# Kernel tuning notes

Hardware: AMD Instinct MI355X
Metric: run time of the kernel (lower is better)

## Reference

```python
import jax, jax.numpy as jnp
import numpy as np
from jax import lax

B, L, D_MODEL = 2, 4096, 1024
D_INNER = 2 * D_MODEL          # expand=2
D_STATE = D_INNER              # required: complex einsum contracts d_inner vs d_state
DT_RANK = 64                   # ceil(1024/16)
D_CONV = 4


def setup_inputs() -> dict:
    key = jax.random.key(0)
    ks = jax.random.split(key, 16)
    s = lambda *sh: 1.0 / np.sqrt(sh[-1])
    return {
        "hidden_states": jax.random.normal(ks[0], (B, L, D_MODEL), jnp.float32),
        "delta": jax.random.normal(ks[1], (B, L, DT_RANK), jnp.float32),
        # in_proj: Linear(d_model -> 2*d_inner), no bias
        "in_proj_w": jax.random.normal(ks[2], (2 * D_INNER, D_MODEL), jnp.float32) * s(D_MODEL),
        # depthwise causal conv1d: (out=d_inner, in/groups=1, k)
        "conv_w": jax.random.normal(ks[3], (D_INNER, 1, D_CONV), jnp.float32) * s(D_CONV),
        "conv_b": jax.random.normal(ks[4], (D_INNER,), jnp.float32) * 0.01,
        # ComplexStateSpace: only A_real affects the real output (x is real)
        "A_real": jax.random.normal(ks[5], (D_STATE, D_STATE), jnp.float32) * 0.1 / np.sqrt(D_STATE),
        # MIMO linears (torch Linear weight layout [out, in])
        "B_w": jax.random.normal(ks[6], (D_STATE, D_INNER), jnp.float32) * 0.1 * s(D_INNER),
        "C_w": jax.random.normal(ks[7], (D_INNER, D_STATE), jnp.float32) * 0.1 * s(D_STATE),
        "D_w": jax.random.normal(ks[8], (D_INNER, D_INNER), jnp.float32) * 0.1 * s(D_INNER),
        # SelectiveScan params
        "dt_proj_w": jax.random.normal(ks[9], (D_INNER, DT_RANK), jnp.float32) * 0.01,
        "dt_proj_b": jax.random.normal(ks[10], (D_INNER,), jnp.float32) * 0.01,
        "A_log": jax.random.uniform(ks[11], (D_INNER,), jnp.float32, -4.0, -1.0),
        "D_ss": jnp.ones((D_INNER,), jnp.float32),
        # out_proj: Linear(d_inner -> d_model), no bias
        "out_proj_w": jax.random.normal(ks[12], (D_MODEL, D_INNER), jnp.float32) * s(D_INNER),
    }


def reference(hidden_states, delta, in_proj_w, conv_w, conv_b, A_real,
              B_w, C_w, D_w, dt_proj_w, dt_proj_b, A_log, D_ss, out_proj_w):
    d_inner = A_log.shape[0]
    # in_proj + split
    xz = jnp.einsum('bld,ed->ble', hidden_states, in_proj_w)
    x, z = xz[..., :d_inner], xz[..., d_inner:]
    # depthwise causal conv1d (left-pad k-1 == torch pad both + truncate to L)
    xc = jnp.swapaxes(x, 1, 2)                      # [b, d, l]
    xc = lax.conv_general_dilated(xc, conv_w, window_strides=(1,),
                                  padding=[(D_CONV - 1, 0)],
                                  feature_group_count=d_inner)
    x = jnp.swapaxes(xc, 1, 2) + conv_b             # [b, l, d]
    x = jax.nn.silu(x)
    # ComplexStateSpace: real part of (x @ (A_real + iA_imag)) == x @ A_real
    x = x + jnp.einsum('bls,st->blt', x, A_real)
    # MIMO SSM: state_t = cumsum(B x)_t ; y_t = C state_t + D x_t  (vectorized)
    Bx = jnp.einsum('bld,sd->bls', x, B_w)          # [b, l, d_state]
    states = jnp.cumsum(Bx, axis=1)
    x_mimo = jnp.einsum('bls,es->ble', states, C_w) + jnp.einsum('bld,ed->ble', x, D_w)
    x = x + x_mimo
    # SelectiveScan: state = state * exp(dlt * A) + u, A = -exp(A_log)
    dlt = jax.nn.softplus(jnp.einsum('blr,dr->bld', delta, dt_proj_w) + dt_proj_b)
    decay = jnp.exp(dlt * (-jnp.exp(A_log)))        # [b, l, d], in (0, 1)

    def step(state, inp):
        dec, u = inp
        state = state * dec + u
        return state, state

    init = jnp.zeros_like(x[:, 0])
    _, scan_states = lax.scan(step, init,
                              (jnp.swapaxes(decay, 0, 1), jnp.swapaxes(x, 0, 1)))
    x = jnp.swapaxes(scan_states, 0, 1) + x * D_ss
    # gate + out projection
    out = x * jax.nn.silu(z)
    return jnp.einsum('ble,de->bld', out, out_proj_w)
```

## Files before the change

kernel.cpp:

```cpp
#include <hip/hip_runtime.h>
#include <cstdint>
#include <cstddef>


typedef unsigned short u16;
typedef __bf16 bf16x8 __attribute__((ext_vector_type(8)));
typedef float  f32x4  __attribute__((ext_vector_type(4)));

#define BDIM 256
#define M_ROWS 8192
#define LSEQ   4096
#define DI     2048
#define NCH    64
#define CLEN   64

__device__ __forceinline__ float bf2f(u16 h) {
    return __uint_as_float(((unsigned int)h) << 16);
}
__device__ __forceinline__ u16 f2bf(float f) {
    unsigned int u = __float_as_uint(f);
    u = u + 0x7fffu + ((u >> 16) & 1u);
    return (u16)(u >> 16);
}
__device__ __forceinline__ float siluf(float v) { return v / (1.0f + __expf(-v)); }

__device__ __forceinline__ void load16_to_lds(const u16* g, u16* l) {
    __builtin_amdgcn_global_load_lds((const __attribute__((address_space(1))) void*)g,
                                     (__attribute__((address_space(3))) void*)l,
                                     16, 0, 0);
}

__global__ void k_cvt_all(const float* __restrict__ hs, const float* __restrict__ inproj,
                          const float* __restrict__ Bw, const float* __restrict__ Cw,
                          const float* __restrict__ outw, const float* __restrict__ delta,
                          const float* __restrict__ dtw, const float* __restrict__ Areal,
                          const float* __restrict__ Dw, const float* __restrict__ Alog,
                          u16* __restrict__ XH, u16* __restrict__ W1, u16* __restrict__ WBb,
                          u16* __restrict__ WC, u16* __restrict__ WO, u16* __restrict__ DLT,
                          u16* __restrict__ WDT, u16* __restrict__ Pb, u16* __restrict__ Db,
                          float* __restrict__ NA) {
    long i = (long)(blockIdx.x * BDIM + threadIdx.x) * 4;
    if (i >= 32112640L) {
        long j = i - 32112640L;
        if (j < 2048) {
            float4 v = *reinterpret_cast<const float4*>(Alog + j);
            float4 o = {-__expf(v.x), -__expf(v.y), -__expf(v.z), -__expf(v.w)};
            *reinterpret_cast<float4*>(NA + j) = o;
        }
        return;
    }
    const float* src; u16* dst; long off; bool diag = false;
    if      (i <  8388608L) { src = hs;     dst = XH;  off = 0L; }
    else if (i < 12582912L) { src = inproj; dst = W1;  off = 8388608L; }
    else if (i < 16777216L) { src = Bw;     dst = WBb; off = 12582912L; }
    else if (i < 20971520L) { src = Cw;     dst = WC;  off = 16777216L; }
    else if (i < 23068672L) { src = outw;   dst = WO;  off = 20971520L; }
    else if (i < 23592960L) { src = delta;  dst = DLT; off = 23068672L; }
    else if (i < 23724032L) { src = dtw;    dst = WDT; off = 23592960L; }
    else if (i < 27918336L) { src = Areal;  dst = Pb;  off = 23724032L; diag = true; }
    else                    { src = Dw;     dst = Db;  off = 27918336L; diag = true; }
    long j = i - off;
    float4 v = *reinterpret_cast<const float4*>(src + j);
    if (diag) {
        int r = (int)(j >> 11), c = (int)(j & 2047);
        if (r >= c && r < c + 4) (&v.x)[r - c] += 1.0f;
    }
    ushort2 a = {f2bf(v.x), f2bf(v.y)};
    ushort2 b = {f2bf(v.z), f2bf(v.w)};
    *reinterpret_cast<ushort2*>(dst + j)     = a;
    *reinterpret_cast<ushort2*>(dst + j + 2) = b;
}

__device__ __forceinline__ void gemm_core(
    u16* As, u16* Bs,
    const u16* __restrict__ A1, const u16* __restrict__ W1, int K1,
    const u16* __restrict__ A2, const u16* __restrict__ W2, int K2,
    int N, float* __restrict__ outf, u16* __restrict__ outb, u16* __restrict__ outb2,
    const float* __restrict__ bias1, const float* __restrict__ bias2,
    int m0, int n0, int mode) {
    const int tid  = threadIdx.x;
    const int wave = tid >> 6;
    const int lane = tid & 63;
    const int wm = (wave >> 1) * 64;
    const int wn = (wave & 1) * 64;
    const int lr = lane & 15;
    const int lq = lane >> 4;
    const int stg_row = lane >> 3;
    const int stg_col = (((lane & 7) ^ (lane >> 3)) << 3);

    f32x4 acc[4][4] = {};

    const int nt1 = K1 >> 6;
    const int nt2 = K2 >> 6;
    const int ntot = nt1 + nt2;

    for (int kt = 0; kt < ntot; ++kt) {
        const u16* Ap; const u16* Wp; int ld, k0;
        if (kt < nt1) { Ap = A1; Wp = W1; ld = K1; k0 = kt << 6; }
        else          { Ap = A2; Wp = W2; ld = K2; k0 = (kt - nt1) << 6; }
        #pragma unroll
        for (int i = 0; i < 4; ++i) {
            int chunk = wave * 4 + i;
            int r = chunk * 8 + stg_row;
            load16_to_lds(Ap + (size_t)(m0 + r) * ld + (k0 + stg_col), As + chunk * 512);
            load16_to_lds(Wp + (size_t)(n0 + r) * ld + (k0 + stg_col), Bs + chunk * 512);
        }
        __syncthreads();
        #pragma unroll
        for (int kk = 0; kk < 64; kk += 32) {
            bf16x8 af[4], bfr[4];
            #pragma unroll
            for (int i = 0; i < 4; ++i) {
                int R = wm + i * 16 + lr;
                af[i] = *reinterpret_cast<const bf16x8*>(
                    &As[R * 64 + ((kk + lq * 8) ^ ((R & 7) << 3))]);
            }
            #pragma unroll
            for (int i = 0; i < 4; ++i) {
                int R = wn + i * 16 + lr;
                bfr[i] = *reinterpret_cast<const bf16x8*>(
                    &Bs[R * 64 + ((kk + lq * 8) ^ ((R & 7) << 3))]);
            }
            #pragma unroll
            for (int mi = 0; mi < 4; ++mi)
                #pragma unroll
                for (int ni = 0; ni < 4; ++ni)
                    acc[mi][ni] = __builtin_amdgcn_mfma_f32_16x16x32_bf16(
                        af[mi], bfr[ni], acc[mi][ni], 0, 0, 0);
        }
        __syncthreads();
    }

    if (mode == 8) {
        #pragma unroll
        for (int mi = 0; mi < 4; ++mi) {
            #pragma unroll
            for (int ni = 0; ni < 4; ++ni) {
                int row = m0 + wm + mi * 16 + lq * 4;
                int col = n0 + wn + ni * 16 + lr;
                ushort4 v;
                v.x = f2bf(acc[mi][ni][0]); v.y = f2bf(acc[mi][ni][1]);
                v.z = f2bf(acc[mi][ni][2]); v.w = f2bf(acc[mi][ni][3]);
                *reinterpret_cast<ushort4*>(outb + (size_t)col * 2048 + row) = v;
            }
        }
        return;
    }

    #pragma unroll
    for (int mi = 0; mi < 4; ++mi) {
        #pragma unroll
        for (int ni = 0; ni < 4; ++ni) {
            #pragma unroll
            for (int j = 0; j < 4; ++j) {
                int row = m0 + wm + mi * 16 + lq * 4 + j;
                int col = n0 + wn + ni * 16 + lr;
                float v = acc[mi][ni][j];
                if (mode == 6) {
                    if (col < 2048) outb [(size_t)row * 2048 + col]        = f2bf(v);
                    else            outb2[(size_t)row * 2048 + col - 2048] = f2bf(v);
                } else if (mode == 5) {
                    float dlt = v + bias1[col];
                    float sp  = (dlt > 15.f) ? dlt : __logf(1.f + __expf(dlt));
                    outb[(size_t)row * N + col] = f2bf(bias2[col] * sp);
                } else if (mode == 2) {
                    outf[(size_t)row * N + col] = v;
                } else {
                    outb[(size_t)row * N + col] = f2bf(v);
                }
            }
        }
    }
}

__device__ __forceinline__ void tile_coords(int q, int T, int gn, int& m0, int& n0) {
    int xcd  = q & 7;
    int loc  = q >> 3;
    int SM   = (T >> 3) / gn;
    int CH   = gn < 8 ? gn : 8;
    int span = SM * CH;
    int chunk = loc / span;
    int rem   = loc - chunk * span;
    int ml    = rem / CH;
    int nl    = rem - ml * CH;
    m0 = (xcd * SM + ml) * 128;
    n0 = (chunk * CH + nl) * 128;
}

__global__ __launch_bounds__(256, 4)
void k_batch1(const u16* __restrict__ XH, const u16* __restrict__ W1,
              const u16* __restrict__ WBb, const u16* __restrict__ Pb,
              const u16* __restrict__ Db,
              u16* __restrict__ PBt, u16* __restrict__ WXp,
              u16* __restrict__ XB, u16* __restrict__ ZB) {
    __shared__ u16 As[128 * 64];
    __shared__ u16 Bs[128 * 64];
    int bid = blockIdx.x;
    int m0, n0;
    if (bid < 256) {
        tile_coords(bid, 256, 16, m0, n0);
        gemm_core(As, Bs, Pb, WBb, DI, nullptr, nullptr, 0, DI,
                  nullptr, PBt, nullptr, nullptr, nullptr, m0, n0, 0);
    } else if (bid < 512) {
        tile_coords(bid - 256, 256, 16, m0, n0);
        gemm_core(As, Bs, Db, Pb, DI, nullptr, nullptr, 0, DI,
                  nullptr, WXp, nullptr, nullptr, nullptr, m0, n0, 0);
    } else {
        tile_coords(bid - 512, 2048, 32, m0, n0);
        gemm_core(As, Bs, XH, W1, 1024, nullptr, nullptr, 0, 4096,
                  nullptr, XB, ZB, nullptr, nullptr, m0, n0, 6);
    }
}

__global__ __launch_bounds__(256, 4)
void k_conv_pre3(const u16* __restrict__ x, const float* __restrict__ w,
                 const float* __restrict__ b, u16* __restrict__ out,
                 const u16* __restrict__ PBt, const u16* __restrict__ WC,
                 u16* __restrict__ WCBp,
                 const u16* __restrict__ DLT, const u16* __restrict__ WDT,
                 const float* __restrict__ dtb, const float* __restrict__ NA,
                 u16* __restrict__ LD) {
    __shared__ u16 As[128 * 64];
    __shared__ u16 Bs[128 * 64];
    if (blockIdx.x < 256) {
        int m0, n0;
        tile_coords(blockIdx.x, 256, 16, m0, n0);
        gemm_core(As, Bs, PBt, WC, DI, nullptr, nullptr, 0, DI,
                  nullptr, WCBp, nullptr, nullptr, nullptr, m0, n0, 8);
        return;
    }
    if (blockIdx.x < 1280) {
        int m0, n0;
        tile_coords(blockIdx.x - 256, 1024, 16, m0, n0);
        gemm_core(As, Bs, DLT, WDT, 64, nullptr, nullptr, 0, DI,
                  nullptr, LD, nullptr, dtb, NA, m0, n0, 5);
        return;
    }
    int idx = (blockIdx.x - 1280) * BDIM + threadIdx.x;
    int d  = idx & (DI - 1);
    int bl = idx >> 11;
    int l  = bl & (LSEQ - 1);
    float4 wv = *reinterpret_cast<const float4*>(w + d * 4);
    float wj[4] = {wv.x, wv.y, wv.z, wv.w};
    float acc = b[d];
    #pragma unroll
    for (int j = 0; j < 4; ++j) {
        int ll = l - 3 + j;
        if (ll >= 0) acc += wj[j] * bf2f(x[(size_t)(bl - 3 + j) * DI + d]);
    }
    out[idx] = f2bf(siluf(acc));
}

__global__ __launch_bounds__(512, 2)
void k_g36(const u16* __restrict__ A, const u16* __restrict__ W,
           u16* __restrict__ BXC, u16* __restrict__ X3) {
    __shared__ u16 As[2][256 * 64];
    __shared__ u16 Bs[2][256 * 64];
    const int tid  = threadIdx.x;
    const int wave = tid >> 6;
    const int lane = tid & 63;
    const int wm = (wave >> 2) * 128;
    const int wn = (wave & 3) * 64;
    const int lr = lane & 15;
    const int lq = lane >> 4;
    const int stg_row = lane >> 3;
    const int stg_col = (((lane & 7) ^ (lane >> 3)) << 3);

    int q    = blockIdx.x;
    int xcd  = q & 7;
    int loc  = q >> 3;
    int chnk = loc >> 5;
    int rem  = loc & 31;
    int ml   = rem >> 3, nl = rem & 7;
    int m0 = (xcd * 4 + ml) * 256;
    int n0 = (chnk * 8 + nl) * 256;

    const int K = 2048;
    const int nt = 32;

    f32x4 acc[8][4] = {};

    auto stage = [&](int kt) {
        int c  = kt & 1;
        int k0 = kt << 6;
        #pragma unroll
        for (int i = 0; i < 4; ++i) {
            int ch = wave * 4 + i;
            int r  = ch * 8 + stg_row;
            load16_to_lds(A + (size_t)(m0 + r) * K + (k0 + stg_col), &As[c][ch * 512]);
            load16_to_lds(W + (size_t)(n0 + r) * K + (k0 + stg_col), &Bs[c][ch * 512]);
        }
    };
    auto rdA = [&](const u16* as, int kk, bf16x8 (&dst)[8]) {
        #pragma unroll
        for (int mi = 0; mi < 8; ++mi) {
            int R = wm + mi * 16 + lr;
            dst[mi] = *reinterpret_cast<const bf16x8*>(
                &as[R * 64 + ((kk + lq * 8) ^ ((R & 7) << 3))]);
        }
    };
    auto rdB = [&](const u16* bs, int kk, bf16x8 (&dst)[4]) {
        #pragma unroll
        for (int ni = 0; ni < 4; ++ni) {
            int R = wn + ni * 16 + lr;
            dst[ni] = *reinterpret_cast<const bf16x8*>(
                &bs[R * 64 + ((kk + lq * 8) ^ ((R & 7) << 3))]);
        }
    };
    auto mfma16 = [&](bf16x8 (&a)[8], bf16x8 (&b)[4]) {
        #pragma unroll
        for (int mi = 0; mi < 8; ++mi)
            #pragma unroll
            for (int ni = 0; ni < 4; ++ni)
                acc[mi][ni] = __builtin_amdgcn_mfma_f32_16x16x32_bf16(
                    a[mi], b[ni], acc[mi][ni], 0, 0, 0);
    };

    stage(0);
    stage(1);
    asm volatile("s_waitcnt vmcnt(8)" ::: "memory");
    __builtin_amdgcn_s_barrier();

    bf16x8 af[8], bfr[4], af2[8], bfr2[4];
    rdA(&As[0][0], 0, af);
    rdB(&Bs[0][0], 0, bfr);

    for (int kt = 0; kt < nt - 1; ++kt) {
        const u16* as  = &As[kt & 1][0];
        const u16* bs  = &Bs[kt & 1][0];
        const u16* asn = &As[(kt + 1) & 1][0];
        const u16* bsn = &Bs[(kt + 1) & 1][0];
        mfma16(af, bfr);
        rdA(as, 32, af2);
        rdB(bs, 32, bfr2);
        asm volatile("s_waitcnt lgkmcnt(0)" ::: "memory");
        __builtin_amdgcn_sched_barrier(0);
        __builtin_amdgcn_s_barrier();
        if (kt + 2 < nt) {
            stage(kt + 2);
            asm volatile("s_waitcnt vmcnt(8)" ::: "memory");
        } else {
            asm volatile("s_waitcnt vmcnt(0)" ::: "memory");
        }
        __builtin_amdgcn_s_barrier();
        __builtin_amdgcn_s_setprio(1);
        mfma16(af2, bfr2);
        rdA(asn, 0, af);
        rdB(bsn, 0, bfr);
        __builtin_amdgcn_s_setprio(0);
    }
    {
        const u16* as = &As[(nt - 1) & 1][0];
        const u16* bs = &Bs[(nt - 1) & 1][0];
        mfma16(af, bfr);
        rdA(as, 32, af2);
        rdB(bs, 32, bfr2);
        mfma16(af2, bfr2);
    }

    u16* ob = (n0 < 2048) ? BXC : X3;
    int nb  = n0 & 2047;
    #pragma unroll
    for (int mi = 0; mi < 8; ++mi)
        #pragma unroll
        for (int ni = 0; ni < 4; ++ni)
            #pragma unroll
            for (int j = 0; j < 4; ++j) {
                int row = m0 + wm + mi * 16 + lq * 4 + j;
                int col = nb + wn + ni * 16 + lr;
                ob[(size_t)row * 2048 + col] = f2bf(acc[mi][ni][j]);
            }
}

template <int MODE>
__global__ __launch_bounds__(256, 4)
void k_gemm(const u16* __restrict__ A1, const u16* __restrict__ W1, int K1,
            const u16* __restrict__ A2, const u16* __restrict__ W2, int K2,
            int N, float* __restrict__ outf, u16* __restrict__ outb) {
    __shared__ u16 As[128 * 64];
    __shared__ u16 Bs[128 * 64];
    int bid = blockIdx.x + gridDim.x * blockIdx.y;
    int m0, n0;
    tile_coords(bid, gridDim.x * gridDim.y, gridDim.x, m0, n0);
    gemm_core(As, Bs, A1, W1, K1, A2, W2, K2, N,
              outf, outb, nullptr, nullptr, nullptr, m0, n0, MODE);
}

__global__ void k_cumsum_p1(const u16* __restrict__ Bx, float* __restrict__ aux) {
    int t = blockIdx.x * BDIM + threadIdx.x;
    int s = t & (DI - 1);
    int c = (t >> 11) & (NCH - 1);
    int b = t >> 17;
    const u16* p = Bx + ((size_t)(b * LSEQ + c * CLEN) * DI) + s;
    float sum = 0.f;
    for (int i = 0; i < CLEN; ++i) sum += bf2f(p[(size_t)i * DI]);
    aux[t] = sum;
}
__global__ void k_cs23_scan1(const u16* __restrict__ Bx, const float* __restrict__ aux,
                             u16* x3, const u16* __restrict__ ld_,
                             float* __restrict__ auxA, float* __restrict__ auxS) {
    int t = blockIdx.x * BDIM + threadIdx.x;
    int s = t & (DI - 1);
    int c = (t >> 11) & (NCH - 1);
    int b = t >> 17;
    float run = 0.f;
    for (int j = 0; j < c; ++j) run += aux[(b * NCH + j) * DI + s];
    size_t base = ((size_t)(b * LSEQ + c * CLEN) * DI) + s;
    float ap = 1.f, sc = 0.f;
    for (int i = 0; i < CLEN; ++i) {
        size_t ix = base + (size_t)i * DI;
        run += bf2f(Bx[ix]);
        u16 xb = f2bf(run + bf2f(x3[ix]));
        x3[ix] = xb;
        float a = __expf(bf2f(ld_[ix]));
        sc = fmaf(a, sc, bf2f(xb));
        ap *= a;
    }
    auxA[t] = ap; auxS[t] = sc;
}

__global__ void k_scan_p23(const u16* __restrict__ ld_, const u16* __restrict__ u,
                           const float* __restrict__ auxA, const float* __restrict__ auxS,
                           const u16* __restrict__ z, const float* __restrict__ Dss,
                           u16* __restrict__ outb) {
    int t = blockIdx.x * BDIM + threadIdx.x;
    int d = t & (DI - 1);
    int c = (t >> 11) & (NCH - 1);
    int b = t >> 17;
    float s = 0.f;
    for (int j = 0; j < c; ++j) {
        int i = (b * NCH + j) * DI + d;
        s = fmaf(auxA[i], s, auxS[i]);
    }
    size_t base = ((size_t)(b * LSEQ + c * CLEN) * DI) + d;
    float dss = Dss[d];
    for (int i = 0; i < CLEN; ++i) {
        size_t ix = base + (size_t)i * DI;
        float a = __expf(bf2f(ld_[ix]));
        float uu = bf2f(u[ix]);
        s = fmaf(a, s, uu);
        float x4 = s + uu * dss;
        float zz = bf2f(z[ix]);
        outb[ix] = f2bf(x4 * siluf(zz));
    }
}

extern "C" void kernel_launch(void* const* d_in, const int* in_sizes, int n_in,
                              void* d_out, int out_size, void* d_ws, size_t ws_size,
                              hipStream_t stream) {
    const float* hs     = (const float*)d_in[0];
    const float* delta  = (const float*)d_in[1];
    const float* inproj = (const float*)d_in[2];
    const float* convw  = (const float*)d_in[3];
    const float* convb  = (const float*)d_in[4];
    const float* Areal  = (const float*)d_in[5];
    const float* Bw     = (const float*)d_in[6];
    const float* Cw     = (const float*)d_in[7];
    const float* Dw     = (const float*)d_in[8];
    const float* dtw    = (const float*)d_in[9];
    const float* dtb    = (const float*)d_in[10];
    const float* Alog   = (const float*)d_in[11];
    const float* Dss    = (const float*)d_in[12];
    const float* outw   = (const float*)d_in[13];
    float* out = (float*)d_out;

    const size_t SZ_ACT = (size_t)M_ROWS * DI * 2;
    char* p = (char*)d_ws;
    u16* ZB  = (u16*)p; p += SZ_ACT;
    u16* XB  = (u16*)p;
    u16* X3  = XB;      p += SZ_ACT;
    u16* XC  = (u16*)p;
    u16* OUT = XC;      p += SZ_ACT;
    u16* BXC = (u16*)p; p += SZ_ACT;
    u16* WCBp= (u16*)p;
    u16* WXp = WCBp + (size_t)DI * DI;
                        p += SZ_ACT;
    u16* XH  = (u16*)p;
    u16* LD  = XH;
                        p += (size_t)M_ROWS * 1024 * 2;
    u16* W1  = (u16*)p; p += (size_t)4096 * 1024 * 2;
    u16* WBb = (u16*)p; p += (size_t)DI * DI * 2;
    u16* WC  = (u16*)p; p += (size_t)DI * DI * 2;
    u16* Pb  = (u16*)p; p += (size_t)DI * DI * 2;
    u16* Db  = (u16*)p; p += (size_t)DI * DI * 2;
    u16* PBt = (u16*)p; p += (size_t)DI * DI * 2;
    p += (size_t)DI * DI * 2;
    u16* WO  = (u16*)p; p += (size_t)1024 * DI * 2;
    u16* WDT = (u16*)p; p += (size_t)DI * 64 * 2;
    u16* DLT = (u16*)p; p += (size_t)M_ROWS * 64 * 2;
    float* aux1 = (float*)p; p += (size_t)2 * NCH * DI * 4;
    float* auxA = (float*)p; p += (size_t)2 * NCH * DI * 4;
    float* auxS = (float*)p; p += (size_t)2 * NCH * DI * 4;
    float* NA   = (float*)p; p += (size_t)DI * 4;

    k_cvt_all<<<31362, BDIM, 0, stream>>>(hs, inproj, Bw, Cw, outw, delta, dtw,
                                          Areal, Dw, Alog,
                                          XH, W1, WBb, WC, WO, DLT, WDT, Pb, Db, NA);
    k_batch1<<<2560, BDIM, 0, stream>>>(XH, W1, WBb, Pb, Db, PBt, WXp, XB, ZB);
    k_conv_pre3<<<1280 + (M_ROWS * DI) / BDIM, BDIM, 0, stream>>>(
        XB, convw, convb, XC, PBt, WC, WCBp, DLT, WDT, dtb, NA, LD);
    k_g36<<<512, 512, 0, stream>>>(XC, WCBp, BXC, X3);
    k_cumsum_p1<<<(2 * NCH * DI) / BDIM, BDIM, 0, stream>>>(BXC, aux1);
    k_cs23_scan1<<<(2 * NCH * DI) / BDIM, BDIM, 0, stream>>>(BXC, aux1, X3,
                                                             LD, auxA, auxS);
    k_scan_p23<<<(2 * NCH * DI) / BDIM, BDIM, 0, stream>>>(LD, X3, auxA, auxS,
                                                           ZB, Dss, OUT);
    k_gemm<2><<<dim3(8, 64), BDIM, 0, stream>>>(OUT, WO, DI, nullptr, nullptr, 0,
                                                1024, out, nullptr);
}
```

Baseline: 630.0 us.

## Interleave GEMM staging with MFMA phases and fuse chunk sums into epilogue

Restructures the k_g36 main loop into four sub-phases per K tile. Each phase issues a slice of the next tile's global-to-LDS loads while MFMAs run on the current tile. This spreads memory traffic across the compute and changes launch bounds to one block per SM. Separately, the GEMM epilogue now computes the per-64-row chunk column sums of the Bx output with shuffles and writes aux1 directly, so the k_cumsum_p1 kernel and its re-read of Bx are removed. The risks are extra barriers per tile, lower occupancy, and register pressure from the epilogue sums.

```diff
diff --git a/kernel.cpp b/kernel.cpp
--- a/kernel.cpp
+++ b/kernel.cpp
@@ -251,9 +251,9 @@
     out[idx] = f2bf(siluf(acc));
 }
 
-__global__ __launch_bounds__(512, 2)
+__global__ __launch_bounds__(512, 1)
 void k_g36(const u16* __restrict__ A, const u16* __restrict__ W,
-           u16* __restrict__ BXC, u16* __restrict__ X3) {
+           u16* __restrict__ BXC, u16* __restrict__ X3, float* __restrict__ aux1) {
     __shared__ u16 As[2][256 * 64];
     __shared__ u16 Bs[2][256 * 64];
     const int tid  = threadIdx.x;
@@ -280,86 +280,103 @@
 
     f32x4 acc[8][4] = {};
 
-    auto stage = [&](int kt) {
-        int c  = kt & 1;
-        int k0 = kt << 6;
-        #pragma unroll
-        for (int i = 0; i < 4; ++i) {
-            int ch = wave * 4 + i;
-            int r  = ch * 8 + stg_row;
-            load16_to_lds(A + (size_t)(m0 + r) * K + (k0 + stg_col), &As[c][ch * 512]);
-            load16_to_lds(W + (size_t)(n0 + r) * K + (k0 + stg_col), &Bs[c][ch * 512]);
-        }
+    const int a1c0 = 2 * wave,      a1c1 = 2 * wave + 1;
+    const int a2c0 = 16 + 2 * wave, a2c1 = 17 + 2 * wave;
+    const int bk0  = ((wave >> 1) << 3) + ((wave & 1) << 1);
+    const int b1c0 = bk0,     b1c1 = bk0 + 1;
+    const int b2c0 = bk0 + 4, b2c1 = bk0 + 5;
+
+    auto stgA = [&](int wb, int k0, int ch) {
+        load16_to_lds(A + (size_t)(m0 + ch * 8 + stg_row) * K + (k0 + stg_col),
+                      &As[wb][ch * 512]);
     };
-    auto rdA = [&](const u16* as, int kk, bf16x8 (&dst)[8]) {
+    auto stgB = [&](int wb, int k0, int ch) {
+        load16_to_lds(W + (size_t)(n0 + ch * 8 + stg_row) * K + (k0 + stg_col),
+                      &Bs[wb][ch * 512]);
+    };
+    auto rdA8 = [&](const u16* as_, int kk, bf16x8 (&dst)[8]) {
         #pragma unroll
         for (int mi = 0; mi < 8; ++mi) {
             int R = wm + mi * 16 + lr;
             dst[mi] = *reinterpret_cast<const bf16x8*>(
-                &as[R * 64 + ((kk + lq * 8) ^ ((R & 7) << 3))]);
+                &as_[R * 64 + ((kk + lq * 8) ^ ((R & 7) << 3))]);
         }
     };
-    auto rdB = [&](const u16* bs, int kk, bf16x8 (&dst)[4]) {
-        #pragma unroll
-        for (int ni = 0; ni < 4; ++ni) {
-            int R = wn + ni * 16 + lr;
-            dst[ni] = *reinterpret_cast<const bf16x8*>(
-                &bs[R * 64 + ((kk + lq * 8) ^ ((R & 7) << 3))]);
-        }
+    auto rdB1 = [&](const u16* bs_, int kk, int ni, bf16x8& d) {
+        int R = wn + ni * 16 + lr;
+        d = *reinterpret_cast<const bf16x8*>(
+            &bs_[R * 64 + ((kk + lq * 8) ^ ((R & 7) << 3))]);
     };
-    auto mfma16 = [&](bf16x8 (&a)[8], bf16x8 (&b)[4]) {
+    auto mf8 = [&](bf16x8 (&a)[8], bf16x8 b, int ni) {
         #pragma unroll
         for (int mi = 0; mi < 8; ++mi)
-            #pragma unroll
-            for (int ni = 0; ni < 4; ++ni)
-                acc[mi][ni] = __builtin_amdgcn_mfma_f32_16x16x32_bf16(
-                    a[mi], b[ni], acc[mi][ni], 0, 0, 0);
+            acc[mi][ni] = __builtin_amdgcn_mfma_f32_16x16x32_bf16(
+                a[mi], b, acc[mi][ni], 0, 0, 0);
     };
 
-    stage(0);
-    stage(1);
-    asm volatile("s_waitcnt vmcnt(8)" ::: "memory");
+    stgA(0, 0, a1c0); stgA(0, 0, a1c1); stgA(0, 0, a2c0); stgA(0, 0, a2c1);
+    stgB(0, 0, b1c0); stgB(0, 0, b1c1); stgB(0, 0, b2c0); stgB(0, 0, b2c1);
+    asm volatile("s_waitcnt vmcnt(0)" ::: "memory");
     __builtin_amdgcn_s_barrier();
 
-    bf16x8 af[8], bfr[4], af2[8], bfr2[4];
-    rdA(&As[0][0], 0, af);
-    rdB(&Bs[0][0], 0, bfr);
-
-    for (int kt = 0; kt < nt - 1; ++kt) {
-        const u16* as  = &As[kt & 1][0];
-        const u16* bs  = &Bs[kt & 1][0];
-        const u16* asn = &As[(kt + 1) & 1][0];
-        const u16* bsn = &Bs[(kt + 1) & 1][0];
-        mfma16(af, bfr);
-        rdA(as, 32, af2);
-        rdB(bs, 32, bfr2);
+    for (int kt = 0; kt < nt; ++kt) {
+        const u16* as_ = &As[kt & 1][0];
+        const u16* bs_ = &Bs[kt & 1][0];
+        const int  wb  = (kt + 1) & 1;
+        const int  k1  = (kt + 1) << 6;
+        const bool st  = (kt + 1 < nt);
+        bf16x8 af[8], b0, b1, b2, b3;
+
+        rdA8(as_, 0, af);
+        rdB1(bs_, 0, 0, b0); rdB1(bs_, 0, 1, b1);
+        if (st) { stgA(wb, k1, a1c0); stgA(wb, k1, a1c1); }
+        __builtin_amdgcn_s_barrier();
         asm volatile("s_waitcnt lgkmcnt(0)" ::: "memory");
         __builtin_amdgcn_sched_barrier(0);
-        __builtin_amdgcn_s_barrier();
-        if (kt + 2 < nt) {
-            stage(kt + 2);
-            asm volatile("s_waitcnt vmcnt(8)" ::: "memory");
-        } else {
-            asm volatile("s_waitcnt vmcnt(0)" ::: "memory");
-        }
-        __builtin_amdgcn_s_barrier();
         __builtin_amdgcn_s_setprio(1);
-        mfma16(af2, bfr2);
-        rdA(asn, 0, af);
-        rdB(bsn, 0, bfr);
+        mf8(af, b0, 0); mf8(af, b1, 1);
         __builtin_amdgcn_s_setprio(0);
-    }
-    {
-        const u16* as = &As[(nt - 1) & 1][0];
-        const u16* bs = &Bs[(nt - 1) & 1][0];
-        mfma16(af, bfr);
-        rdA(as, 32, af2);
-        rdB(bs, 32, bfr2);
-        mfma16(af2, bfr2);
-    }
-
-    u16* ob = (n0 < 2048) ? BXC : X3;
-    int nb  = n0 & 2047;
+        if (st) { asm volatile("s_waitcnt vmcnt(2)" ::: "memory"); }
+        else    { asm volatile("s_waitcnt vmcnt(0)" ::: "memory"); }
+        __builtin_amdgcn_s_barrier();
+
+        rdB1(bs_, 0, 2, b2); rdB1(bs_, 0, 3, b3);
+        if (st) { stgA(wb, k1, a2c0); stgA(wb, k1, a2c1); }
+        __builtin_amdgcn_s_barrier();
+        asm volatile("s_waitcnt lgkmcnt(0)" ::: "memory");
+        __builtin_amdgcn_sched_barrier(0);
+        __builtin_amdgcn_s_setprio(1);
+        mf8(af, b2, 2); mf8(af, b3, 3);
+        __builtin_amdgcn_s_setprio(0);
+        __builtin_amdgcn_s_barrier();
+
+        rdA8(as_, 32, af);
+        rdB1(bs_, 32, 0, b0); rdB1(bs_, 32, 1, b1);
+        if (st) { stgB(wb, k1, b1c0); stgB(wb, k1, b1c1); }
+        __builtin_amdgcn_s_barrier();
+        asm volatile("s_waitcnt lgkmcnt(0)" ::: "memory");
+        __builtin_amdgcn_sched_barrier(0);
+        __builtin_amdgcn_s_setprio(1);
+        mf8(af, b0, 0); mf8(af, b1, 1);
+        __builtin_amdgcn_s_setprio(0);
+        __builtin_amdgcn_s_barrier();
+
+        rdB1(bs_, 32, 2, b2); rdB1(bs_, 32, 3, b3);
+        if (st) { stgB(wb, k1, b2c0); stgB(wb, k1, b2c1); }
+        __builtin_amdgcn_s_barrier();
+        asm volatile("s_waitcnt lgkmcnt(0)" ::: "memory");
+        __builtin_amdgcn_sched_barrier(0);
+        __builtin_amdgcn_s_setprio(1);
+        mf8(af, b2, 2); mf8(af, b3, 3);
+        __builtin_amdgcn_s_setprio(0);
+        if (st) { asm volatile("s_waitcnt vmcnt(2)" ::: "memory"); }
+        __builtin_amdgcn_s_barrier();
+    }
+
+    const bool isB = (n0 < 2048);
+    u16* ob = isB ? BXC : X3;
+    const int nb = n0 & 2047;
+    float cs[2][4] = {};
     #pragma unroll
     for (int mi = 0; mi < 8; ++mi)
         #pragma unroll
@@ -368,8 +385,27 @@
             for (int j = 0; j < 4; ++j) {
                 int row = m0 + wm + mi * 16 + lq * 4 + j;
                 int col = nb + wn + ni * 16 + lr;
-                ob[(size_t)row * 2048 + col] = f2bf(acc[mi][ni][j]);
+                u16 r = f2bf(acc[mi][ni][j]);
+                ob[(size_t)row * 2048 + col] = r;
+                if (isB) cs[mi >> 2][ni] += bf2f(r);
             }
+    if (isB) {
+        #pragma unroll
+        for (int g = 0; g < 2; ++g)
+            #pragma unroll
+            for (int ni = 0; ni < 4; ++ni) {
+                float v = cs[g][ni];
+                v += __shfl_xor(v, 16);
+                v += __shfl_xor(v, 32);
+                if (lq == 0) {
+                    int rowbase = m0 + wm + g * 64;
+                    int bb = rowbase >> 12;
+                    int cc = (rowbase & (LSEQ - 1)) >> 6;
+                    int col = nb + wn + ni * 16 + lr;
+                    aux1[(size_t)(bb * NCH + cc) * DI + col] = v;
+                }
+            }
+    }
 }
 
 template <int MODE>
@@ -386,16 +422,6 @@
               outf, outb, nullptr, nullptr, nullptr, m0, n0, MODE);
 }
 
-__global__ void k_cumsum_p1(const u16* __restrict__ Bx, float* __restrict__ aux) {
-    int t = blockIdx.x * BDIM + threadIdx.x;
-    int s = t & (DI - 1);
-    int c = (t >> 11) & (NCH - 1);
-    int b = t >> 17;
-    const u16* p = Bx + ((size_t)(b * LSEQ + c * CLEN) * DI) + s;
-    float sum = 0.f;
-    for (int i = 0; i < CLEN; ++i) sum += bf2f(p[(size_t)i * DI]);
-    aux[t] = sum;
-}
 __global__ void k_cs23_scan1(const u16* __restrict__ Bx, const float* __restrict__ aux,
                              u16* x3, const u16* __restrict__ ld_,
                              float* __restrict__ auxA, float* __restrict__ auxS) {
@@ -499,8 +525,7 @@
     k_batch1<<<2560, BDIM, 0, stream>>>(XH, W1, WBb, Pb, Db, PBt, WXp, XB, ZB);
     k_conv_pre3<<<1280 + (M_ROWS * DI) / BDIM, BDIM, 0, stream>>>(
         XB, convw, convb, XC, PBt, WC, WCBp, DLT, WDT, dtb, NA, LD);
-    k_g36<<<512, 512, 0, stream>>>(XC, WCBp, BXC, X3);
-    k_cumsum_p1<<<(2 * NCH * DI) / BDIM, BDIM, 0, stream>>>(BXC, aux1);
+    k_g36<<<512, 512, 0, stream>>>(XC, WCBp, BXC, X3, aux1);
     k_cs23_scan1<<<(2 * NCH * DI) / BDIM, BDIM, 0, stream>>>(BXC, aux1, X3,
                                                              LD, auxA, auxS);
     k_scan_p23<<<(2 * NCH * DI) / BDIM, BDIM, 0, stream>>>(LD, X3, auxA, auxS,
```

After: 649.1 us. 1.03x slower.
